# Kernel tuning notes

Measured on AMD Instinct MI355X. Metric: run time of the kernel, lower is better.

Reference implementation:

```python
import jax, jax.numpy as jnp
import numpy as np

THRES1 = 0.8      # self.thres1
THRES_UP = 0.5    # self.thres_up
R = 1.0           # self.r
MAX_FRAME = 60    # self.max_frame
SEQ, FEAT = 65536, 512


def _get_thres2(max_frame=MAX_FRAME, thres=0.6):
    # Faithful port of TGNN.get_threshold: grid-search alpha in (0,1] step 0.01
    a = 0.0
    e = 0.01
    min_score = 1e7
    alpha = e
    for _ in range(100):
        a = a + e
        y = 0.0
        for _ in range(max_frame):
            y = a * 1.0 + (1.0 - a) * y
        score = abs(y - thres)
        if min_score > score:
            min_score = score
            alpha = a
    # with up=1, a_ stays == alpha, so y[i] = alpha + (1-alpha)*y[i-1]
    y = 0.0
    ys = []
    for _ in range(max_frame):
        y = alpha + (1.0 - alpha) * y
        ys.append(y)
    return np.asarray(ys, dtype=np.float32)


def setup_inputs() -> dict:
    key = jax.random.key(0)
    k0, k1, k2, k3, k4 = jax.random.split(key, 5)
    h = jax.random.normal(k0, (SEQ, FEAT), jnp.float32)            # per-frame CTR features
    W = jax.random.normal(k1, (FEAT, 1), jnp.float32) / np.float32(np.sqrt(FEAT))
    b = jnp.zeros((1,), jnp.float32)
    u = jax.random.uniform(k2, (SEQ,), jnp.float32)                # batch['u'] (unused in loss, as in torch)
    u_pred = jax.random.uniform(k3, (SEQ,), jnp.float32)           # batch['u_pred']
    label = jax.random.uniform(k4, (SEQ,), jnp.float32)            # batch['y']
    thres2 = jnp.asarray(_get_thres2())
    return {"h": h, "W": W, "b": b, "u": u, "u_pred": u_pred, "label": label, "thres2": thres2}


def reference(h, W, b, u, u_pred, label, thres2):
    # stand-in for self.ctr.calc_alpha(h).squeeze(): per-frame alpha in (0,1)
    a = jax.nn.sigmoid(h @ W + b)[:, 0]                             # [seq]
    seq = a.shape[0]
    idxs = jnp.arange(seq, dtype=jnp.int32)

    def step(carry, xs):
        up_pre, up_max, a_pre, y_pre, l_c, loss, cnt = carry
        i, a_i, up_i, lab_i = xs
        # start_frame is reset to 0 at the top of every torch iteration, so
        # i - start_frame == 0 whenever start_frame > 0 -> that elif never fires,
        # and in the l_e branch start_frame == 0 -> index is simply i.
        cross = (up_pre < THRES_UP) & (up_i >= THRES_UP)
        up_max = jnp.where(cross, up_i, jnp.maximum(up_max, up_i))
        up_hat = jnp.where(up_i >= THRES_UP, up_max, up_i)
        alpha_ = up_hat * a_pre + (1.0 - up_hat) * a_i
        y_ = alpha_ * up_hat + (1.0 - alpha_) * y_pre
        y_ = jnp.where(up_hat < THRES_UP, jnp.float32(0.0), y_)
        # label >= thres1: set pending loss l_c (sentinel -1 if gate closed)
        l_c = jnp.where(lab_i >= THRES1,
                        jnp.where(up_hat < THRES_UP, jnp.float32(-1.0), (y_ - lab_i) ** 2),
                        l_c)
        # falling edge of the gate: flush accumulated loss
        fall = (up_pre >= THRES_UP) & (up_hat < THRES_UP)
        is_neg = l_c == -1.0
        nonzero = l_c != 0.0
        t2 = thres2[jnp.minimum(i, MAX_FRAME - 1)]
        l_e = (y_pre - t2) ** 2
        add_c = fall & (~is_neg) & nonzero
        add_e = fall & (~is_neg) & (~nonzero) & (y_pre >= THRES1)
        loss = loss + jnp.where(add_c, l_c * R, 0.0) + jnp.where(add_e, l_e, 0.0)
        cnt = cnt + (add_c | add_e).astype(jnp.int32)
        l_c = jnp.where(fall, jnp.float32(0.0), l_c)
        return (up_hat, up_max, alpha_, y_, l_c, loss, cnt), (alpha_, up_hat, y_)

    z = jnp.float32(0.0)
    init = (z, z, z, z, z, z, jnp.int32(0))
    (_, _, _, _, _, loss, cnt), (alphas, up_hats, ys) = jax.lax.scan(
        step, init, (idxs, a, u_pred, label))
    return ys, alphas, u_pred, up_hats, loss, cnt
```

## Files before the change

### kernel.cpp

```cpp
#include <hip/hip_runtime.h>
#include <math.h>

#define SEQ 65536
#define FEAT 512
#define NCH 256
#define CHUNK 256
#define THRES1 0.8f
#define THRES_UP 0.5f
#define NEGINF -1e30f

__global__ __launch_bounds__(256) void k_matvec_local(
        const float* __restrict__ h, const float* __restrict__ W,
        const float* __restrict__ b, const float* __restrict__ u_pred,
        const float* __restrict__ label,
        float* __restrict__ a,
        float* __restrict__ m_loc, int* __restrict__ openA,
        int* __restrict__ ltLoc, int* __restrict__ lfExcl,
        float* __restrict__ lastm, int* __restrict__ lastopen,
        int* __restrict__ lastgate, int* __restrict__ trigLast,
        int* __restrict__ fallLast, float* __restrict__ losscnt) {
    {
        int wave = threadIdx.x >> 6;
        int lane = threadIdx.x & 63;
        int g    = lane >> 4;
        int s    = lane & 15;
        int row  = blockIdx.x * 16 + wave * 4 + g;
        const float4* hp = (const float4*)(h + (size_t)row * FEAT);
        const float4* wp = (const float4*)W;
        float4 h0 = hp[s],       h1 = hp[s + 16],  h2 = hp[s + 32],  h3 = hp[s + 48];
        float4 h4 = hp[s + 64],  h5 = hp[s + 80],  h6 = hp[s + 96],  h7 = hp[s + 112];
        float4 w0 = wp[s],       w1 = wp[s + 16],  w2 = wp[s + 32],  w3 = wp[s + 48];
        float4 w4 = wp[s + 64],  w5 = wp[s + 80],  w6 = wp[s + 96],  w7 = wp[s + 112];
        float bb = b[0];
        float acc0 = h0.x * w0.x + h0.y * w0.y + h0.z * w0.z + h0.w * w0.w
                   + h2.x * w2.x + h2.y * w2.y + h2.z * w2.z + h2.w * w2.w
                   + h4.x * w4.x + h4.y * w4.y + h4.z * w4.z + h4.w * w4.w
                   + h6.x * w6.x + h6.y * w6.y + h6.z * w6.z + h6.w * w6.w;
        float acc1 = h1.x * w1.x + h1.y * w1.y + h1.z * w1.z + h1.w * w1.w
                   + h3.x * w3.x + h3.y * w3.y + h3.z * w3.z + h3.w * w3.w
                   + h5.x * w5.x + h5.y * w5.y + h5.z * w5.z + h5.w * w5.w
                   + h7.x * w7.x + h7.y * w7.y + h7.z * w7.z + h7.w * w7.w;
        float acc = acc0 + acc1;
        #pragma unroll
        for (int m = 8; m; m >>= 1) acc += __shfl_xor(acc, m, 64);
        if (s == 0) a[row] = 1.0f / (1.0f + expf(-(acc + bb)));
    }
    if (blockIdx.x == 0 && threadIdx.x == 0) { losscnt[0] = 0.0f; losscnt[1] = 0.0f; }
    if (blockIdx.x < NCH) {
        __shared__ float su[256];
        __shared__ float sm[256];
        __shared__ int   sr[256];
        __shared__ int   st[256];
        __shared__ int   sf[256];
        int t = threadIdx.x, c = blockIdx.x;
        int i = c * CHUNK + t;
        float u = u_pred[i];
        su[t] = u;
        __syncthreads();
        bool gate = u >= THRES_UP;
        bool gprevLocal = (t > 0) && (su[t - 1] >= THRES_UP);
        bool gprev = (t > 0) ? gprevLocal : ((i > 0) && (u_pred[i - 1] >= THRES_UP));
        bool fall = gprev && !gate;
        bool trig = label[i] >= THRES1;

        sm[t] = gate ? u : NEGINF;
        sr[t] = gate ? ((t > 0 && !gprevLocal) ? 1 : 0) : 1;
        st[t] = trig ? i : -1;
        sf[t] = fall ? i : -1;
        __syncthreads();
        for (int d = 1; d < 256; d <<= 1) {
            float lm = NEGINF; int lr = 0, lt = -1, lf = -1;
            bool act = t >= d;
            if (act) { lm = sm[t - d]; lr = sr[t - d]; lt = st[t - d]; lf = sf[t - d]; }
            __syncthreads();
            if (act) {
                if (!sr[t]) sm[t] = fmaxf(lm, sm[t]);
                sr[t] |= lr;
                st[t] = max(st[t], lt);
                sf[t] = max(sf[t], lf);
            }
            __syncthreads();
        }
        m_loc[i]  = sm[t];
        openA[i]  = (sr[t] == 0 && gate) ? 1 : 0;
        ltLoc[i]  = st[t];
        lfExcl[i] = (t == 0) ? -1 : sf[t - 1];
        if (t == 255) {
            lastm[c]    = sm[255];
            lastopen[c] = (sr[255] == 0 && gate) ? 1 : 0;
            lastgate[c] = gate ? 1 : 0;
            trigLast[c] = st[255];
            fallLast[c] = sf[255];
        }
    }
}

__global__ __launch_bounds__(256) void k_uphat_alpha(
        const float* __restrict__ u_pred, const float* __restrict__ a,
        const float* __restrict__ m_loc, const int* __restrict__ openA,
        const float* __restrict__ lastm, const int* __restrict__ lastopen,
        const int* __restrict__ lastgate,
        float* __restrict__ Pc, float* __restrict__ Qc,
        float* __restrict__ Pch, float* __restrict__ Qch,
        float* __restrict__ out) {
    __shared__ float sc[256], sd[256];
    int t = threadIdx.x, c = blockIdx.x;
    int i = c * CHUNK + t;

    {
        bool lg = lastgate[t] != 0;
        sc[t] = lg ? lastm[t] : NEGINF;
        sd[t] = (lg && lastopen[t]) ? 0.0f : NEGINF;
    }
    __syncthreads();
    for (int d = 1; d < 256; d <<= 1) {
        float lA = NEGINF, lB = NEGINF;
        bool act = t >= d;
        if (act) { lA = sc[t - d]; lB = sd[t - d]; }
        __syncthreads();
        if (act) {
            float nA = fmaxf(sc[t], sd[t] + lA);
            float nB = fmaxf(sd[t] + lB, NEGINF);
            sc[t] = nA; sd[t] = nB;
        }
        __syncthreads();
    }
    float inc_c = (c == 0) ? NEGINF : sc[c - 1];
    __syncthreads();

    float u = u_pred[i];
    bool gate = u >= THRES_UP;
    float uh = gate ? (openA[i] ? fmaxf(m_loc[i], inc_c) : m_loc[i]) : u;
    out[3 * SEQ + i] = uh;
    out[2 * SEQ + i] = u;
    sc[t] = uh;
    sd[t] = (1.0f - uh) * a[i];
    __syncthreads();
    for (int d = 1; d < 256; d <<= 1) {
        float lc = 1.0f, ld = 0.0f;
        bool act = t >= d;
        if (act) { lc = sc[t - d]; ld = sd[t - d]; }
        __syncthreads();
        if (act) { sd[t] = sc[t] * ld + sd[t]; sc[t] = sc[t] * lc; }
        __syncthreads();
    }
    Pc[i] = sc[t];
    Qc[i] = sd[t];
    if (t == 255) { Pch[c] = sc[255]; Qch[c] = sd[255]; }
}

__global__ __launch_bounds__(256) void k_alpha_y(
        float* __restrict__ Pc, float* __restrict__ Qc,
        const float* __restrict__ Pch, const float* __restrict__ Qch,
        float* __restrict__ out,
        float* __restrict__ Ech, float* __restrict__ Fch) {
    __shared__ float sc[256], sd[256];
    int t = threadIdx.x, c = blockIdx.x;
    int i = c * CHUNK + t;

    sc[t] = Pch[t]; sd[t] = Qch[t];
    __syncthreads();
    for (int d = 1; d < 256; d <<= 1) {
        float lc = 1.0f, ld = 0.0f;
        bool act = t >= d;
        if (act) { lc = sc[t - d]; ld = sd[t - d]; }
        __syncthreads();
        if (act) { sd[t] = sc[t] * ld + sd[t]; sc[t] = sc[t] * lc; }
        __syncthreads();
    }
    float alphaIn_c = (c == 0) ? 0.0f : sd[c - 1];
    __syncthreads();

    float al = Pc[i] * alphaIn_c + Qc[i];
    out[SEQ + i] = al;
    float uh = out[3 * SEQ + i];
    bool gate = uh >= THRES_UP;
    sc[t] = gate ? (1.0f - al) : 0.0f;
    sd[t] = gate ? al * uh : 0.0f;
    __syncthreads();
    for (int d = 1; d < 256; d <<= 1) {
        float lc = 1.0f, ld = 0.0f;
        bool act = t >= d;
        if (act) { lc = sc[t - d]; ld = sd[t - d]; }
        __syncthreads();
        if (act) { sd[t] = sc[t] * ld + sd[t]; sc[t] = sc[t] * lc; }
        __syncthreads();
    }
    Pc[i] = sc[t];
    Qc[i] = sd[t];
    if (t == 255) { Ech[c] = sc[255]; Fch[c] = sd[255]; }
}

__global__ __launch_bounds__(256) void k_yfinal_loss(
        const float* __restrict__ Ec, const float* __restrict__ Fc,
        const float* __restrict__ Ech, const float* __restrict__ Fch,
        const int* __restrict__ trigLast, const int* __restrict__ fallLast,
        const float* __restrict__ u_pred, const float* __restrict__ label,
        const float* __restrict__ thres2,
        const int* __restrict__ ltLoc, const int* __restrict__ lfExcl,
        float* __restrict__ out) {
    __shared__ float sc[256], sd[256], syIn[256];
    __shared__ int   st[256], sf[256];
    int t = threadIdx.x, c = blockIdx.x;
    int i = c * CHUNK + t;

    sc[t] = Ech[t]; sd[t] = Fch[t];
    st[t] = trigLast[t]; sf[t] = fallLast[t];
    __syncthreads();
    for (int d = 1; d < 256; d <<= 1) {
        float lc = 1.0f, ld = 0.0f; int lt = -1, lf = -1;
        bool act = t >= d;
        if (act) { lc = sc[t - d]; ld = sd[t - d]; lt = st[t - d]; lf = sf[t - d]; }
        __syncthreads();
        if (act) {
            sd[t] = sc[t] * ld + sd[t]; sc[t] = sc[t] * lc;
            st[t] = max(st[t], lt);
            sf[t] = max(sf[t], lf);
        }
        __syncthreads();
    }
    syIn[t] = (t == 0) ? 0.0f : sd[t - 1];
    int trigIn_c = (c == 0) ? -1 : st[c - 1];
    int fallIn_c = (c == 0) ? -1 : sf[c - 1];
    __syncthreads();

    out[i] = Ec[i] * syIn[c] + Fc[i];

    float u = u_pred[i];
    bool gate = u >= THRES_UP;
    bool gprev = (i > 0) && (u_pred[i - 1] >= THRES_UP);
    bool fall = gprev && !gate;
    float contrib = 0.0f;
    int flag = 0;
    if (fall) {
        int j  = max(ltLoc[i], trigIn_c);
        int pf = max(lfExcl[i], fallIn_c);
        float lc = 0.0f;
        if (j > pf) {
            bool gj = u_pred[j] >= THRES_UP;
            float yj = Ec[j] * syIn[j >> 8] + Fc[j];
            float d = yj - label[j];
            lc = gj ? d * d : -1.0f;
        }
        bool isneg = (lc == -1.0f);
        bool nonzero = (lc != 0.0f);
        if (!isneg) {
            if (nonzero) { contrib = lc; flag = 1; }
            else {
                int ip = i - 1;
                float ypre = Ec[ip] * syIn[ip >> 8] + Fc[ip];
                if (ypre >= THRES1) {
                    float t2 = thres2[(i < 59) ? i : 59];
                    float d2 = ypre - t2;
                    contrib = d2 * d2; flag = 1;
                }
            }
        }
    }
    #pragma unroll
    for (int off = 32; off; off >>= 1) {
        contrib += __shfl_down(contrib, off, 64);
        flag    += __shfl_down(flag, off, 64);
    }
    if ((t & 63) == 0 && (contrib != 0.0f || flag != 0)) {
        atomicAdd(&out[4 * SEQ], contrib);
        atomicAdd(&out[4 * SEQ + 1], (float)flag);
    }
}

extern "C" void kernel_launch(void* const* d_in, const int* in_sizes, int n_in,
                              void* d_out, int out_size, void* d_ws, size_t ws_size,
                              hipStream_t stream) {
    const float* h      = (const float*)d_in[0];
    const float* W      = (const float*)d_in[1];
    const float* b      = (const float*)d_in[2];
    const float* u_pred = (const float*)d_in[4];
    const float* label  = (const float*)d_in[5];
    const float* thres2 = (const float*)d_in[6];
    float* out  = (float*)d_out;
    float* base = (float*)d_ws;

    float* a      = base;
    float* m_loc  = base + SEQ;
    float* Pc     = base + 2 * (size_t)SEQ;
    float* Qc     = base + 3 * (size_t)SEQ;
    int*   openA  = (int*)(base + 4 * (size_t)SEQ);
    int*   ltLoc  = (int*)(base + 5 * (size_t)SEQ);
    int*   lfExcl = (int*)(base + 6 * (size_t)SEQ);
    float* sums   = base + 7 * (size_t)SEQ;
    float* lastm   = sums;
    float* Pch     = sums + NCH;
    float* Qch     = sums + 2 * NCH;
    float* Ech     = sums + 3 * NCH;
    float* Fch     = sums + 4 * NCH;
    int*   lastopen = (int*)(sums + 5 * NCH);
    int*   lastgate = (int*)(sums + 6 * NCH);
    int*   trigLast = (int*)(sums + 7 * NCH);
    int*   fallLast = (int*)(sums + 8 * NCH);

    k_matvec_local<<<SEQ / 16, 256, 0, stream>>>(h, W, b, u_pred, label, a,
                                                 m_loc, openA, ltLoc, lfExcl,
                                                 lastm, lastopen, lastgate, trigLast, fallLast,
                                                 out + 4 * SEQ);
    k_uphat_alpha<<<NCH, CHUNK, 0, stream>>>(u_pred, a, m_loc, openA,
                                             lastm, lastopen, lastgate,
                                             Pc, Qc, Pch, Qch, out);
    k_alpha_y<<<NCH, CHUNK, 0, stream>>>(Pc, Qc, Pch, Qch, out, Ech, Fch);
    k_yfinal_loss<<<NCH, CHUNK, 0, stream>>>(Pc, Qc, Ech, Fch, trigLast, fallLast,
                                             u_pred, label, thres2, ltLoc, lfExcl, out);
}
```

Before: 239.0 us.

## Replace shared-memory Hillis-Steele scans with wavefront shuffle scans and use nontemporal loads

Each of the three scan kernels now scans inside a 64-lane wavefront with __shfl_up and combines the four wave totals through a small shared array. This replaces the eight-round shared-memory Hillis-Steele scans that needed two barriers per round. The h rows in the matvec are read with nontemporal loads so the streamed matrix does not pollute cache. The cost is more shuffle instructions, and the floating-point combine order changes slightly.

```diff
diff --git a/kernel.cpp b/kernel.cpp
--- a/kernel.cpp
+++ b/kernel.cpp
@@ -8,6 +8,8 @@
 #define THRES1 0.8f
 #define THRES_UP 0.5f
 #define NEGINF -1e30f
+
+typedef float v4f __attribute__((ext_vector_type(4)));
 
 __global__ __launch_bounds__(256) void k_matvec_local(
         const float* __restrict__ h, const float* __restrict__ W,
@@ -25,12 +27,18 @@
         int g    = lane >> 4;
         int s    = lane & 15;
         int row  = blockIdx.x * 16 + wave * 4 + g;
-        const float4* hp = (const float4*)(h + (size_t)row * FEAT);
-        const float4* wp = (const float4*)W;
-        float4 h0 = hp[s],       h1 = hp[s + 16],  h2 = hp[s + 32],  h3 = hp[s + 48];
-        float4 h4 = hp[s + 64],  h5 = hp[s + 80],  h6 = hp[s + 96],  h7 = hp[s + 112];
-        float4 w0 = wp[s],       w1 = wp[s + 16],  w2 = wp[s + 32],  w3 = wp[s + 48];
-        float4 w4 = wp[s + 64],  w5 = wp[s + 80],  w6 = wp[s + 96],  w7 = wp[s + 112];
+        const v4f* hp = (const v4f*)(h + (size_t)row * FEAT);
+        const v4f* wp = (const v4f*)W;
+        v4f h0 = __builtin_nontemporal_load(hp + s);
+        v4f h1 = __builtin_nontemporal_load(hp + s + 16);
+        v4f h2 = __builtin_nontemporal_load(hp + s + 32);
+        v4f h3 = __builtin_nontemporal_load(hp + s + 48);
+        v4f h4 = __builtin_nontemporal_load(hp + s + 64);
+        v4f h5 = __builtin_nontemporal_load(hp + s + 80);
+        v4f h6 = __builtin_nontemporal_load(hp + s + 96);
+        v4f h7 = __builtin_nontemporal_load(hp + s + 112);
+        v4f w0 = wp[s],       w1 = wp[s + 16],  w2 = wp[s + 32],  w3 = wp[s + 48];
+        v4f w4 = wp[s + 64],  w5 = wp[s + 80],  w6 = wp[s + 96],  w7 = wp[s + 112];
         float bb = b[0];
         float acc0 = h0.x * w0.x + h0.y * w0.y + h0.z * w0.z + h0.w * w0.w
                    + h2.x * w2.x + h2.y * w2.y + h2.z * w2.z + h2.w * w2.w
@@ -103,50 +111,61 @@
         float* __restrict__ Pc, float* __restrict__ Qc,
         float* __restrict__ Pch, float* __restrict__ Qch,
         float* __restrict__ out) {
-    __shared__ float sc[256], sd[256];
+    __shared__ float scanA[256];
+    __shared__ float wA[4], wB[4];
     int t = threadIdx.x, c = blockIdx.x;
+    int lane = t & 63, w = t >> 6;
     int i = c * CHUNK + t;
 
     {
         bool lg = lastgate[t] != 0;
-        sc[t] = lg ? lastm[t] : NEGINF;
-        sd[t] = (lg && lastopen[t]) ? 0.0f : NEGINF;
-    }
-    __syncthreads();
-    for (int d = 1; d < 256; d <<= 1) {
-        float lA = NEGINF, lB = NEGINF;
-        bool act = t >= d;
-        if (act) { lA = sc[t - d]; lB = sd[t - d]; }
-        __syncthreads();
-        if (act) {
-            float nA = fmaxf(sc[t], sd[t] + lA);
-            float nB = fmaxf(sd[t] + lB, NEGINF);
-            sc[t] = nA; sd[t] = nB;
-        }
-        __syncthreads();
-    }
-    float inc_c = (c == 0) ? NEGINF : sc[c - 1];
-    __syncthreads();
+        float A = lg ? lastm[t] : NEGINF;
+        float B = (lg && lastopen[t]) ? 0.0f : NEGINF;
+        #pragma unroll
+        for (int off = 1; off < 64; off <<= 1) {
+            float lA = __shfl_up(A, off, 64);
+            float lB = __shfl_up(B, off, 64);
+            if (lane >= off) { A = fmaxf(A, B + lA); B = fmaxf(B + lB, NEGINF); }
+        }
+        if (lane == 63) { wA[w] = A; wB[w] = B; }
+        __syncthreads();
+        float PA = NEGINF, PB = 0.0f;
+        #pragma unroll
+        for (int ww = 0; ww < 3; ++ww)
+            if (ww < w) { float tA = wA[ww], tB = wB[ww];
+                PA = fmaxf(tA, tB + PA); PB = fmaxf(tB + PB, NEGINF); }
+        A = fmaxf(A, B + PA);
+        scanA[t] = A;
+        __syncthreads();
+    }
+    float inc_c = (c == 0) ? NEGINF : scanA[c - 1];
 
     float u = u_pred[i];
     bool gate = u >= THRES_UP;
     float uh = gate ? (openA[i] ? fmaxf(m_loc[i], inc_c) : m_loc[i]) : u;
     out[3 * SEQ + i] = uh;
     out[2 * SEQ + i] = u;
-    sc[t] = uh;
-    sd[t] = (1.0f - uh) * a[i];
+    float cc = uh;
+    float dd = (1.0f - uh) * a[i];
+    #pragma unroll
+    for (int off = 1; off < 64; off <<= 1) {
+        float lc = __shfl_up(cc, off, 64);
+        float ld = __shfl_up(dd, off, 64);
+        if (lane >= off) { dd = cc * ld + dd; cc = cc * lc; }
+    }
+    if (lane == 63) { wA[w] = cc; wB[w] = dd; }
     __syncthreads();
-    for (int d = 1; d < 256; d <<= 1) {
-        float lc = 1.0f, ld = 0.0f;
-        bool act = t >= d;
-        if (act) { lc = sc[t - d]; ld = sd[t - d]; }
-        __syncthreads();
-        if (act) { sd[t] = sc[t] * ld + sd[t]; sc[t] = sc[t] * lc; }
-        __syncthreads();
-    }
-    Pc[i] = sc[t];
-    Qc[i] = sd[t];
-    if (t == 255) { Pch[c] = sc[255]; Qch[c] = sd[255]; }
+    {
+        float pc = 1.0f, pd = 0.0f;
+        #pragma unroll
+        for (int ww = 0; ww < 3; ++ww)
+            if (ww < w) { float tc = wA[ww], td = wB[ww];
+                pd = tc * pd + td; pc = tc * pc; }
+        dd = cc * pd + dd; cc = cc * pc;
+    }
+    Pc[i] = cc;
+    Qc[i] = dd;
+    if (t == 255) { Pch[c] = cc; Qch[c] = dd; }
 }
 
 __global__ __launch_bounds__(256) void k_alpha_y(
@@ -154,41 +173,58 @@
         const float* __restrict__ Pch, const float* __restrict__ Qch,
         float* __restrict__ out,
         float* __restrict__ Ech, float* __restrict__ Fch) {
-    __shared__ float sc[256], sd[256];
+    __shared__ float scanD[256];
+    __shared__ float wA[4], wB[4];
     int t = threadIdx.x, c = blockIdx.x;
+    int lane = t & 63, w = t >> 6;
     int i = c * CHUNK + t;
 
-    sc[t] = Pch[t]; sd[t] = Qch[t];
-    __syncthreads();
-    for (int d = 1; d < 256; d <<= 1) {
-        float lc = 1.0f, ld = 0.0f;
-        bool act = t >= d;
-        if (act) { lc = sc[t - d]; ld = sd[t - d]; }
-        __syncthreads();
-        if (act) { sd[t] = sc[t] * ld + sd[t]; sc[t] = sc[t] * lc; }
-        __syncthreads();
-    }
-    float alphaIn_c = (c == 0) ? 0.0f : sd[c - 1];
-    __syncthreads();
+    {
+        float cc = Pch[t], dd = Qch[t];
+        #pragma unroll
+        for (int off = 1; off < 64; off <<= 1) {
+            float lc = __shfl_up(cc, off, 64);
+            float ld = __shfl_up(dd, off, 64);
+            if (lane >= off) { dd = cc * ld + dd; cc = cc * lc; }
+        }
+        if (lane == 63) { wA[w] = cc; wB[w] = dd; }
+        __syncthreads();
+        float pc = 1.0f, pd = 0.0f;
+        #pragma unroll
+        for (int ww = 0; ww < 3; ++ww)
+            if (ww < w) { float tc = wA[ww], td = wB[ww];
+                pd = tc * pd + td; pc = tc * pc; }
+        dd = cc * pd + dd;
+        scanD[t] = dd;
+        __syncthreads();
+    }
+    float alphaIn_c = (c == 0) ? 0.0f : scanD[c - 1];
 
     float al = Pc[i] * alphaIn_c + Qc[i];
     out[SEQ + i] = al;
     float uh = out[3 * SEQ + i];
     bool gate = uh >= THRES_UP;
-    sc[t] = gate ? (1.0f - al) : 0.0f;
-    sd[t] = gate ? al * uh : 0.0f;
+    float cc = gate ? (1.0f - al) : 0.0f;
+    float dd = gate ? al * uh : 0.0f;
+    #pragma unroll
+    for (int off = 1; off < 64; off <<= 1) {
+        float lc = __shfl_up(cc, off, 64);
+        float ld = __shfl_up(dd, off, 64);
+        if (lane >= off) { dd = cc * ld + dd; cc = cc * lc; }
+    }
+    if (lane == 63) { wA[w] = cc; wB[w] = dd; }
     __syncthreads();
-    for (int d = 1; d < 256; d <<= 1) {
-        float lc = 1.0f, ld = 0.0f;
-        bool act = t >= d;
-        if (act) { lc = sc[t - d]; ld = sd[t - d]; }
-        __syncthreads();
-        if (act) { sd[t] = sc[t] * ld + sd[t]; sc[t] = sc[t] * lc; }
-        __syncthreads();
-    }
-    Pc[i] = sc[t];
-    Qc[i] = sd[t];
-    if (t == 255) { Ech[c] = sc[255]; Fch[c] = sd[255]; }
+    {
+        float pc = 1.0f, pd = 0.0f;
+        #pragma unroll
+        for (int ww = 0; ww < 3; ++ww)
+            if (ww < w) { float tc = wA[ww], td = wB[ww];
+                pd = tc * pd + td; pc = tc * pc; }
+        dd = cc * pd + dd; cc = cc * pc;
+    }
+    Pc[i] = cc;
+    Qc[i] = dd;
+    if (t == 255) { Ech[c] = cc; Fch[c] = dd; }
 }
 
 __global__ __launch_bounds__(256) void k_yfinal_loss(
@@ -199,32 +235,46 @@
         const float* __restrict__ thres2,
         const int* __restrict__ ltLoc, const int* __restrict__ lfExcl,
         float* __restrict__ out) {
-    __shared__ float sc[256], sd[256], syIn[256];
-    __shared__ int   st[256], sf[256];
+    __shared__ float sdArr[256];
+    __shared__ int   stArr[256], sfArr[256];
+    __shared__ float wC[4], wD[4];
+    __shared__ int   wT[4], wF[4];
     int t = threadIdx.x, c = blockIdx.x;
+    int lane = t & 63, w = t >> 6;
     int i = c * CHUNK + t;
 
-    sc[t] = Ech[t]; sd[t] = Fch[t];
-    st[t] = trigLast[t]; sf[t] = fallLast[t];
-    __syncthreads();
-    for (int d = 1; d < 256; d <<= 1) {
-        float lc = 1.0f, ld = 0.0f; int lt = -1, lf = -1;
-        bool act = t >= d;
-        if (act) { lc = sc[t - d]; ld = sd[t - d]; lt = st[t - d]; lf = sf[t - d]; }
-        __syncthreads();
-        if (act) {
-            sd[t] = sc[t] * ld + sd[t]; sc[t] = sc[t] * lc;
-            st[t] = max(st[t], lt);
-            sf[t] = max(sf[t], lf);
-        }
-        __syncthreads();
-    }
-    syIn[t] = (t == 0) ? 0.0f : sd[t - 1];
-    int trigIn_c = (c == 0) ? -1 : st[c - 1];
-    int fallIn_c = (c == 0) ? -1 : sf[c - 1];
-    __syncthreads();
-
-    out[i] = Ec[i] * syIn[c] + Fc[i];
+    {
+        float cc = Ech[t], dd = Fch[t];
+        int   T = trigLast[t], F = fallLast[t];
+        #pragma unroll
+        for (int off = 1; off < 64; off <<= 1) {
+            float lc = __shfl_up(cc, off, 64);
+            float ld = __shfl_up(dd, off, 64);
+            int   lt = __shfl_up(T, off, 64);
+            int   lf = __shfl_up(F, off, 64);
+            if (lane >= off) {
+                dd = cc * ld + dd; cc = cc * lc;
+                T = max(T, lt); F = max(F, lf);
+            }
+        }
+        if (lane == 63) { wC[w] = cc; wD[w] = dd; wT[w] = T; wF[w] = F; }
+        __syncthreads();
+        float pc = 1.0f, pd = 0.0f; int pT = -1, pF = -1;
+        #pragma unroll
+        for (int ww = 0; ww < 3; ++ww)
+            if (ww < w) { float tc = wC[ww], td = wD[ww];
+                pd = tc * pd + td; pc = tc * pc;
+                pT = max(pT, wT[ww]); pF = max(pF, wF[ww]); }
+        dd = cc * pd + dd;
+        T = max(T, pT); F = max(F, pF);
+        sdArr[t] = dd; stArr[t] = T; sfArr[t] = F;
+        __syncthreads();
+    }
+    int trigIn_c = (c == 0) ? -1 : stArr[c - 1];
+    int fallIn_c = (c == 0) ? -1 : sfArr[c - 1];
+    float yIn_c = (c == 0) ? 0.0f : sdArr[c - 1];
+
+    out[i] = Ec[i] * yIn_c + Fc[i];
 
     float u = u_pred[i];
     bool gate = u >= THRES_UP;
@@ -238,7 +288,9 @@
         float lc = 0.0f;
         if (j > pf) {
             bool gj = u_pred[j] >= THRES_UP;
-            float yj = Ec[j] * syIn[j >> 8] + Fc[j];
+            int cj = j >> 8;
+            float yInj = (cj == 0) ? 0.0f : sdArr[cj - 1];
+            float yj = Ec[j] * yInj + Fc[j];
             float d = yj - label[j];
             lc = gj ? d * d : -1.0f;
         }
@@ -248,7 +300,9 @@
             if (nonzero) { contrib = lc; flag = 1; }
             else {
                 int ip = i - 1;
-                float ypre = Ec[ip] * syIn[ip >> 8] + Fc[ip];
+                int cp = ip >> 8;
+                float yInp = (cp == 0) ? 0.0f : sdArr[cp - 1];
+                float ypre = Ec[ip] * yInp + Fc[ip];
                 if (ypre >= THRES1) {
                     float t2 = thres2[(i < 59) ? i : 59];
                     float d2 = ypre - t2;
```

New measurement: 226.5 us. -5.2%, faster.
